# Optimization experiments

Hardware: AMD Instinct MI355X
Metric: run time of the kernel (lower is better)

## Reference

```python
import jax, jax.numpy as jnp
import numpy as np

RESO = 128

def _prefix_a3(layer, off0):
    # a3[0]=off0; a3[i]=a3[i-1]+2*layer[i-1]+2*layer[i]
    t = jnp.concatenate([jnp.zeros((1,), layer.dtype), 2.0 * layer[:-1] + 2.0 * layer[1:]])
    return off0 + jnp.cumsum(t)

def _prefix_a6(layer, a3):
    # a6[0]=0; a6[i]=a6[i-1]+3*layer[i-1]+layer[i]+2*a3[i-1]
    s = jnp.concatenate([jnp.zeros((1,), layer.dtype), 3.0 * layer[:-1] + layer[1:] + 2.0 * a3[:-1]])
    return jnp.cumsum(s)

def _decode(idx, reso):
    iz = idx % reso                 # selects xLayer channels (0,3)
    iy = (idx // reso) % reso       # selects yLayer channels (1,4)
    ix = idx // (reso * reso)       # selects zLayer channels (2,5)
    return ix, iy, iz

def setup_inputs() -> dict:
    key = jax.random.key(0)
    k1, k2, k3, k4 = jax.random.split(key, 4)
    N = 4194304
    reso = RESO
    ncells = reso ** 3
    renderPointList = jax.random.normal(k1, (N, 3), dtype=jnp.float32) * reso * 0.3 + reso * 0.5
    sdfPointList = jax.random.normal(k2, (N, 3), dtype=jnp.float32) * reso * 0.3 + reso * 0.5
    renderIndexList = jax.random.randint(k3, (N,), 0, ncells, dtype=jnp.int64) if jax.config.jax_enable_x64 else jax.random.randint(k3, (N,), 0, ncells).astype(jnp.int32)
    sdfIndexList = jax.random.randint(k4, (N,), 0, ncells).astype(renderIndexList.dtype)
    xLayer = jnp.ones((reso,), dtype=jnp.float32)
    yLayer = jnp.ones((reso,), dtype=jnp.float32)
    zLayer = jnp.ones((reso,), dtype=jnp.float32)
    c = 1.0 - reso
    offset = jnp.array([2 * c, 2 * c, 2 * c, 3 * c * c - float(reso) ** 2], dtype=jnp.float32)
    return {"renderPointList": renderPointList, "renderIndexList": renderIndexList,
            "sdfPointList": sdfPointList, "sdfIndexList": sdfIndexList,
            "xLayer": xLayer, "yLayer": yLayer, "zLayer": zLayer, "offset": offset}

def reference(renderPointList, renderIndexList, sdfPointList, sdfIndexList, xLayer, yLayer, zLayer, offset):
    reso = xLayer.shape[0]
    xA3 = _prefix_a3(xLayer, offset[0])
    yA4 = _prefix_a3(yLayer, offset[1])
    zA5 = _prefix_a3(zLayer, offset[2])
    xA6 = _prefix_a6(xLayer, xA3)
    yA6 = _prefix_a6(yLayer, yA4)
    zA6 = _prefix_a6(zLayer, zA5)

    # ---- SDF evaluation ----
    ix, iy, iz = _decode(sdfIndexList, reso)
    px, py, pz = sdfPointList[:, 0], sdfPointList[:, 1], sdfPointList[:, 2]
    a0 = xLayer[iz] * px
    a1 = yLayer[iy] * py
    a2 = zLayer[ix] * pz
    a3 = xA3[iz]
    a4 = yA4[iy]
    a5 = zA5[ix]
    a6 = offset[3] + xA6[iz] + yA6[iy] + zA6[ix]
    num = (a0 + a3) * px + (a1 + a4) * py + (a2 + a5) * pz + a6
    den = jnp.sqrt((2 * a0 + a3) ** 2 + (2 * a1 + a4) ** 2 + (2 * a2 + a5) ** 2)
    sdfList = num / den / reso

    # ---- Normal evaluation ----
    jx, jy, jz = _decode(renderIndexList, reso)
    rx, ry, rz = renderPointList[:, 0], renderPointList[:, 1], renderPointList[:, 2]
    nx = 2 * xLayer[jz] * rx + xA3[jz]
    ny = 2 * yLayer[jy] * ry + yA4[jy]
    nz = 2 * zLayer[jx] * rz + zA5[jx]
    n = jnp.stack([nx, ny, nz], axis=1)  # [N,3]
    norm = jnp.sqrt(jnp.sum(n * n, axis=1, keepdims=True))
    normalList = n / jnp.maximum(norm, 1e-12)
    return (sdfList, normalList)
```

## Files before the change

kernel.cpp:

```cpp
#include <hip/hip_runtime.h>

#define RESO 128

__global__ __launch_bounds__(128) void scan_kernel(
    const float* __restrict__ xL, const float* __restrict__ yL,
    const float* __restrict__ zL, const float* __restrict__ off,
    float* __restrict__ ws)
{
    __shared__ float s_wave[4];
    __shared__ float s_a3[RESO];

    const int tid  = threadIdx.x;
    const int lane = tid & 63;
    const int wave = tid >> 6;

    const float* layers[3] = {xL, yL, zL};

    for (int ax = 0; ax < 3; ++ax) {
        const float* L = layers[ax];
        const float li   = L[tid];
        const float lim1 = (tid > 0) ? L[tid - 1] : 0.0f;

        float v = (tid == 0) ? 0.0f : 2.0f * lim1 + 2.0f * li;
        #pragma unroll
        for (int o = 1; o < 64; o <<= 1) {
            float u = __shfl_up(v, o, 64);
            if (lane >= o) v += u;
        }
        if (lane == 63) s_wave[wave] = v;
        __syncthreads();
        if (wave == 1) v += s_wave[0];
        const float a3 = off[ax] + v;
        s_a3[tid] = a3;
        __syncthreads();

        const float a3m1 = (tid > 0) ? s_a3[tid - 1] : 0.0f;
        float w = (tid == 0) ? 0.0f : 3.0f * lim1 + li + 2.0f * a3m1;
        #pragma unroll
        for (int o = 1; o < 64; o <<= 1) {
            float u = __shfl_up(w, o, 64);
            if (lane >= o) w += u;
        }
        if (lane == 63) s_wave[2 + wave] = w;
        __syncthreads();
        if (wave == 1) w += s_wave[2];

        ws[ax * RESO + tid]       = a3;
        ws[(3 + ax) * RESO + tid] = w;
        __syncthreads();
    }
}

__global__ __launch_bounds__(256) void sdf_kernel(
    const float* __restrict__ pts, const int* __restrict__ idx,
    const float* __restrict__ xL, const float* __restrict__ yL,
    const float* __restrict__ zL, const float* __restrict__ ws,
    const float* __restrict__ off, float* __restrict__ out, int N)
{
    __shared__ float tab[9][RESO];
    const int tid = threadIdx.x;
    if (tid < RESO) {
        tab[0][tid] = xL[tid];
        tab[1][tid] = yL[tid];
        tab[2][tid] = zL[tid];
        #pragma unroll
        for (int k = 0; k < 6; ++k) tab[3 + k][tid] = ws[k * RESO + tid];
    }
    __syncthreads();

    const int i = blockIdx.x * blockDim.x + tid;
    if (i >= N) return;

    const float off3 = off[3];
    const int id = idx[i];
    const int iz = id & 127;
    const int iy = (id >> 7) & 127;
    const int ix = (id >> 14) & 127;

    const float px = pts[3 * i + 0];
    const float py = pts[3 * i + 1];
    const float pz = pts[3 * i + 2];

    const float a0 = tab[0][iz] * px;
    const float a1 = tab[1][iy] * py;
    const float a2 = tab[2][ix] * pz;
    const float a3 = tab[3][iz];
    const float a4 = tab[4][iy];
    const float a5 = tab[5][ix];
    const float a6 = off3 + tab[6][iz] + tab[7][iy] + tab[8][ix];

    const float num = (a0 + a3) * px + (a1 + a4) * py + (a2 + a5) * pz + a6;
    const float dx = 2.0f * a0 + a3;
    const float dy = 2.0f * a1 + a4;
    const float dz = 2.0f * a2 + a5;
    const float den = sqrtf(dx * dx + dy * dy + dz * dz);

    out[i] = num / den / (float)RESO;
}

__global__ __launch_bounds__(256) void render_kernel(
    const float* __restrict__ pts, const int* __restrict__ idx,
    const float* __restrict__ xL, const float* __restrict__ yL,
    const float* __restrict__ zL, const float* __restrict__ ws,
    float* __restrict__ out3, int N)
{
    __shared__ float tab[6][RESO];
    const int tid = threadIdx.x;
    if (tid < RESO) {
        tab[0][tid] = xL[tid];
        tab[1][tid] = yL[tid];
        tab[2][tid] = zL[tid];
        #pragma unroll
        for (int k = 0; k < 3; ++k) tab[3 + k][tid] = ws[k * RESO + tid];
    }
    __syncthreads();

    const int i = blockIdx.x * blockDim.x + tid;
    if (i >= N) return;

    const int id = idx[i];
    const int jz = id & 127;
    const int jy = (id >> 7) & 127;
    const int jx = (id >> 14) & 127;

    const float rx = pts[3 * i + 0];
    const float ry = pts[3 * i + 1];
    const float rz = pts[3 * i + 2];

    const float nx = 2.0f * tab[0][jz] * rx + tab[3][jz];
    const float ny = 2.0f * tab[1][jy] * ry + tab[4][jy];
    const float nz = 2.0f * tab[2][jx] * rz + tab[5][jx];

    const float norm = sqrtf(nx * nx + ny * ny + nz * nz);
    const float d = fmaxf(norm, 1e-12f);

    out3[3 * i + 0] = nx / d;
    out3[3 * i + 1] = ny / d;
    out3[3 * i + 2] = nz / d;
}

extern "C" void kernel_launch(void* const* d_in, const int* in_sizes, int n_in,
                              void* d_out, int out_size, void* d_ws, size_t ws_size,
                              hipStream_t stream)
{
    const float* renderPts = (const float*)d_in[0];
    const int*   renderIdx = (const int*)d_in[1];
    const float* sdfPts    = (const float*)d_in[2];
    const int*   sdfIdx    = (const int*)d_in[3];
    const float* xL        = (const float*)d_in[4];
    const float* yL        = (const float*)d_in[5];
    const float* zL        = (const float*)d_in[6];
    const float* off       = (const float*)d_in[7];

    float* ws  = (float*)d_ws;
    float* out = (float*)d_out;

    const int N = in_sizes[1];

    scan_kernel<<<1, 128, 0, stream>>>(xL, yL, zL, off, ws);

    const int block = 256;
    const int grid = (N + block - 1) / block;
    sdf_kernel<<<grid, block, 0, stream>>>(sdfPts, sdfIdx, xL, yL, zL, ws, off, out, N);
    render_kernel<<<grid, block, 0, stream>>>(renderPts, renderIdx, xL, yL, zL, ws, out + N, N);
}
```

Measured before the change: 187.0 us.

## Fuse scan, SDF and normal kernels into one vectorized kernel

Merges the three launches into one kernel in which every block redundantly computes the 128-entry prefix scans into shared memory, then processes both the SDF and normal outputs. Each thread now handles four points using float4/int4 loads and stores, and the remainder is handled by a single tail thread. This removes two kernel launches, the workspace round trip and the scalar strided 3-float accesses, in exchange for each block repeating the scan, which adds several barriers and lowers the number of threads per element.

```diff
diff --git a/kernel.cpp b/kernel.cpp
--- a/kernel.cpp
+++ b/kernel.cpp
@@ -2,141 +2,157 @@
 
 #define RESO 128
 
-__global__ __launch_bounds__(128) void scan_kernel(
+__global__ __launch_bounds__(256) void fused_kernel(
+    const float* __restrict__ renderPts, const int* __restrict__ renderIdx,
+    const float* __restrict__ sdfPts,    const int* __restrict__ sdfIdx,
     const float* __restrict__ xL, const float* __restrict__ yL,
     const float* __restrict__ zL, const float* __restrict__ off,
-    float* __restrict__ ws)
+    float* __restrict__ sdfOut, float* __restrict__ nrmOut, int N)
 {
-    __shared__ float s_wave[4];
+    __shared__ float tab[9][RESO];
     __shared__ float s_a3[RESO];
+    __shared__ float s_tmp[4];
 
     const int tid  = threadIdx.x;
     const int lane = tid & 63;
     const int wave = tid >> 6;
 
-    const float* layers[3] = {xL, yL, zL};
-
     for (int ax = 0; ax < 3; ++ax) {
-        const float* L = layers[ax];
-        const float li   = L[tid];
-        const float lim1 = (tid > 0) ? L[tid - 1] : 0.0f;
-
-        float v = (tid == 0) ? 0.0f : 2.0f * lim1 + 2.0f * li;
-        #pragma unroll
-        for (int o = 1; o < 64; o <<= 1) {
-            float u = __shfl_up(v, o, 64);
-            if (lane >= o) v += u;
+        const float* L = (ax == 0) ? xL : (ax == 1) ? yL : zL;
+        float li = 0.f, lim1 = 0.f, v = 0.f, w = 0.f, a3v = 0.f;
+        if (tid < RESO) {
+            li   = L[tid];
+            lim1 = (tid > 0) ? L[tid - 1] : 0.f;
+            v = (tid == 0) ? 0.f : 2.f * lim1 + 2.f * li;
+            #pragma unroll
+            for (int o = 1; o < 64; o <<= 1) {
+                float u = __shfl_up(v, o, 64);
+                if (lane >= o) v += u;
+            }
+            if (lane == 63) s_tmp[wave] = v;
         }
-        if (lane == 63) s_wave[wave] = v;
         __syncthreads();
-        if (wave == 1) v += s_wave[0];
-        const float a3 = off[ax] + v;
-        s_a3[tid] = a3;
+        if (tid < RESO) {
+            if (wave == 1) v += s_tmp[0];
+            a3v = off[ax] + v;
+            s_a3[tid] = a3v;
+        }
         __syncthreads();
-
-        const float a3m1 = (tid > 0) ? s_a3[tid - 1] : 0.0f;
-        float w = (tid == 0) ? 0.0f : 3.0f * lim1 + li + 2.0f * a3m1;
-        #pragma unroll
-        for (int o = 1; o < 64; o <<= 1) {
-            float u = __shfl_up(w, o, 64);
-            if (lane >= o) w += u;
+        if (tid < RESO) {
+            const float a3m1 = (tid > 0) ? s_a3[tid - 1] : 0.f;
+            w = (tid == 0) ? 0.f : 3.f * lim1 + li + 2.f * a3m1;
+            #pragma unroll
+            for (int o = 1; o < 64; o <<= 1) {
+                float u = __shfl_up(w, o, 64);
+                if (lane >= o) w += u;
+            }
+            if (lane == 63) s_tmp[2 + wave] = w;
         }
-        if (lane == 63) s_wave[2 + wave] = w;
         __syncthreads();
-        if (wave == 1) w += s_wave[2];
-
-        ws[ax * RESO + tid]       = a3;
-        ws[(3 + ax) * RESO + tid] = w;
+        if (tid < RESO) {
+            if (wave == 1) w += s_tmp[2];
+            tab[ax][tid]     = li;
+            tab[3 + ax][tid] = a3v;
+            tab[6 + ax][tid] = w;
+        }
         __syncthreads();
     }
-}
-
-__global__ __launch_bounds__(256) void sdf_kernel(
-    const float* __restrict__ pts, const int* __restrict__ idx,
-    const float* __restrict__ xL, const float* __restrict__ yL,
-    const float* __restrict__ zL, const float* __restrict__ ws,
-    const float* __restrict__ off, float* __restrict__ out, int N)
-{
-    __shared__ float tab[9][RESO];
-    const int tid = threadIdx.x;
-    if (tid < RESO) {
-        tab[0][tid] = xL[tid];
-        tab[1][tid] = yL[tid];
-        tab[2][tid] = zL[tid];
-        #pragma unroll
-        for (int k = 0; k < 6; ++k) tab[3 + k][tid] = ws[k * RESO + tid];
-    }
-    __syncthreads();
-
-    const int i = blockIdx.x * blockDim.x + tid;
-    if (i >= N) return;
 
     const float off3 = off[3];
-    const int id = idx[i];
-    const int iz = id & 127;
-    const int iy = (id >> 7) & 127;
-    const int ix = (id >> 14) & 127;
+    const int Ng = N >> 2;
+    const int t  = blockIdx.x * blockDim.x + tid;
 
-    const float px = pts[3 * i + 0];
-    const float py = pts[3 * i + 1];
-    const float pz = pts[3 * i + 2];
+    if (t < Ng) {
+        const int4   sid = ((const int4*)sdfIdx)[t];
+        const float4 sp0 = ((const float4*)sdfPts)[3 * t + 0];
+        const float4 sp1 = ((const float4*)sdfPts)[3 * t + 1];
+        const float4 sp2 = ((const float4*)sdfPts)[3 * t + 2];
+        const float px[4] = {sp0.x, sp0.w, sp1.z, sp2.y};
+        const float py[4] = {sp0.y, sp1.x, sp1.w, sp2.z};
+        const float pz[4] = {sp0.z, sp1.y, sp2.x, sp2.w};
+        const int  ids[4] = {sid.x, sid.y, sid.z, sid.w};
 
-    const float a0 = tab[0][iz] * px;
-    const float a1 = tab[1][iy] * py;
-    const float a2 = tab[2][ix] * pz;
-    const float a3 = tab[3][iz];
-    const float a4 = tab[4][iy];
-    const float a5 = tab[5][ix];
-    const float a6 = off3 + tab[6][iz] + tab[7][iy] + tab[8][ix];
+        float sv[4];
+        #pragma unroll
+        for (int k = 0; k < 4; ++k) {
+            const int id = ids[k];
+            const int iz = id & 127;
+            const int iy = (id >> 7) & 127;
+            const int ix = (id >> 14) & 127;
+            const float a0 = tab[0][iz] * px[k];
+            const float a1 = tab[1][iy] * py[k];
+            const float a2 = tab[2][ix] * pz[k];
+            const float a3 = tab[3][iz];
+            const float a4 = tab[4][iy];
+            const float a5 = tab[5][ix];
+            const float a6 = off3 + tab[6][iz] + tab[7][iy] + tab[8][ix];
+            const float num = (a0 + a3) * px[k] + (a1 + a4) * py[k] + (a2 + a5) * pz[k] + a6;
+            const float dx = 2.f * a0 + a3;
+            const float dy = 2.f * a1 + a4;
+            const float dz = 2.f * a2 + a5;
+            const float den = sqrtf(dx * dx + dy * dy + dz * dz);
+            sv[k] = num / den * (1.0f / (float)RESO);
+        }
+        ((float4*)sdfOut)[t] = make_float4(sv[0], sv[1], sv[2], sv[3]);
 
-    const float num = (a0 + a3) * px + (a1 + a4) * py + (a2 + a5) * pz + a6;
-    const float dx = 2.0f * a0 + a3;
-    const float dy = 2.0f * a1 + a4;
-    const float dz = 2.0f * a2 + a5;
-    const float den = sqrtf(dx * dx + dy * dy + dz * dz);
+        const int4   rid = ((const int4*)renderIdx)[t];
+        const float4 rp0 = ((const float4*)renderPts)[3 * t + 0];
+        const float4 rp1 = ((const float4*)renderPts)[3 * t + 1];
+        const float4 rp2 = ((const float4*)renderPts)[3 * t + 2];
+        const float rx[4] = {rp0.x, rp0.w, rp1.z, rp2.y};
+        const float ry[4] = {rp0.y, rp1.x, rp1.w, rp2.z};
+        const float rz[4] = {rp0.z, rp1.y, rp2.x, rp2.w};
+        const int  jds[4] = {rid.x, rid.y, rid.z, rid.w};
 
-    out[i] = num / den / (float)RESO;
-}
+        float nx[4], ny[4], nz[4];
+        #pragma unroll
+        for (int k = 0; k < 4; ++k) {
+            const int id = jds[k];
+            const int jz = id & 127;
+            const int jy = (id >> 7) & 127;
+            const int jx = (id >> 14) & 127;
+            float x = 2.f * tab[0][jz] * rx[k] + tab[3][jz];
+            float y = 2.f * tab[1][jy] * ry[k] + tab[4][jy];
+            float z = 2.f * tab[2][jx] * rz[k] + tab[5][jx];
+            const float nrm = sqrtf(x * x + y * y + z * z);
+            const float inv = 1.0f / fmaxf(nrm, 1e-12f);
+            nx[k] = x * inv; ny[k] = y * inv; nz[k] = z * inv;
+        }
+        float4* no = (float4*)nrmOut;
+        no[3 * t + 0] = make_float4(nx[0], ny[0], nz[0], nx[1]);
+        no[3 * t + 1] = make_float4(ny[1], nz[1], nx[2], ny[2]);
+        no[3 * t + 2] = make_float4(nz[2], nx[3], ny[3], nz[3]);
+    }
 
-__global__ __launch_bounds__(256) void render_kernel(
-    const float* __restrict__ pts, const int* __restrict__ idx,
-    const float* __restrict__ xL, const float* __restrict__ yL,
-    const float* __restrict__ zL, const float* __restrict__ ws,
-    float* __restrict__ out3, int N)
-{
-    __shared__ float tab[6][RESO];
-    const int tid = threadIdx.x;
-    if (tid < RESO) {
-        tab[0][tid] = xL[tid];
-        tab[1][tid] = yL[tid];
-        tab[2][tid] = zL[tid];
-        #pragma unroll
-        for (int k = 0; k < 3; ++k) tab[3 + k][tid] = ws[k * RESO + tid];
+    const int rem = N & 3;
+    if (rem && t == Ng) {
+        for (int r = 0; r < rem; ++r) {
+            const int i = 4 * Ng + r;
+            {
+                const int id = sdfIdx[i];
+                const int iz = id & 127, iy = (id >> 7) & 127, ix = (id >> 14) & 127;
+                const float px_ = sdfPts[3 * i], py_ = sdfPts[3 * i + 1], pz_ = sdfPts[3 * i + 2];
+                const float a0 = tab[0][iz] * px_;
+                const float a1 = tab[1][iy] * py_;
+                const float a2 = tab[2][ix] * pz_;
+                const float a3 = tab[3][iz], a4 = tab[4][iy], a5 = tab[5][ix];
+                const float a6 = off3 + tab[6][iz] + tab[7][iy] + tab[8][ix];
+                const float num = (a0 + a3) * px_ + (a1 + a4) * py_ + (a2 + a5) * pz_ + a6;
+                const float dx = 2.f * a0 + a3, dy = 2.f * a1 + a4, dz = 2.f * a2 + a5;
+                sdfOut[i] = num / sqrtf(dx * dx + dy * dy + dz * dz) * (1.0f / (float)RESO);
+            }
+            {
+                const int id = renderIdx[i];
+                const int jz = id & 127, jy = (id >> 7) & 127, jx = (id >> 14) & 127;
+                const float rx_ = renderPts[3 * i], ry_ = renderPts[3 * i + 1], rz_ = renderPts[3 * i + 2];
+                float x = 2.f * tab[0][jz] * rx_ + tab[3][jz];
+                float y = 2.f * tab[1][jy] * ry_ + tab[4][jy];
+                float z = 2.f * tab[2][jx] * rz_ + tab[5][jx];
+                const float inv = 1.0f / fmaxf(sqrtf(x * x + y * y + z * z), 1e-12f);
+                nrmOut[3 * i] = x * inv; nrmOut[3 * i + 1] = y * inv; nrmOut[3 * i + 2] = z * inv;
+            }
+        }
     }
-    __syncthreads();
-
-    const int i = blockIdx.x * blockDim.x + tid;
-    if (i >= N) return;
-
-    const int id = idx[i];
-    const int jz = id & 127;
-    const int jy = (id >> 7) & 127;
-    const int jx = (id >> 14) & 127;
-
-    const float rx = pts[3 * i + 0];
-    const float ry = pts[3 * i + 1];
-    const float rz = pts[3 * i + 2];
-
-    const float nx = 2.0f * tab[0][jz] * rx + tab[3][jz];
-    const float ny = 2.0f * tab[1][jy] * ry + tab[4][jy];
-    const float nz = 2.0f * tab[2][jx] * rz + tab[5][jx];
-
-    const float norm = sqrtf(nx * nx + ny * ny + nz * nz);
-    const float d = fmaxf(norm, 1e-12f);
-
-    out3[3 * i + 0] = nx / d;
-    out3[3 * i + 1] = ny / d;
-    out3[3 * i + 2] = nz / d;
 }
 
 extern "C" void kernel_launch(void* const* d_in, const int* in_sizes, int n_in,
@@ -152,15 +168,15 @@
     const float* zL        = (const float*)d_in[6];
     const float* off       = (const float*)d_in[7];
 
-    float* ws  = (float*)d_ws;
     float* out = (float*)d_out;
-
     const int N = in_sizes[1];
 
-    scan_kernel<<<1, 128, 0, stream>>>(xL, yL, zL, off, ws);
+    const int Ng    = N >> 2;
+    const int rem   = N & 3;
+    const int total = Ng + (rem ? 1 : 0);
+    int grid = (total + 255) / 256;
+    if (grid < 1) grid = 1;
 
-    const int block = 256;
-    const int grid = (N + block - 1) / block;
-    sdf_kernel<<<grid, block, 0, stream>>>(sdfPts, sdfIdx, xL, yL, zL, ws, off, out, N);
-    render_kernel<<<grid, block, 0, stream>>>(renderPts, renderIdx, xL, yL, zL, ws, out + N, N);
+    fused_kernel<<<grid, 256, 0, stream>>>(renderPts, renderIdx, sdfPts, sdfIdx,
+                                           xL, yL, zL, off, out, out + N, N);
 }
```

New measurement: 189.2 us. About the same (+1.2%).
